# Kernel optimization log

Hardware: AMD Instinct MI355X
Metric: run time of the kernel (lower is better)

## Reference

```python
import jax, jax.numpy as jnp
import numpy as np

N = 4096
INPUT_DIM = 256
HID = 64        # per-head dim == hidden_dim
HEADS = 4
OUT = 256
AIN = 2 * HID   # hidden + positional concat


def sinusoidal_pe(n, d):
    pos = jnp.arange(n, dtype=jnp.float32)[:, None]
    div = jnp.exp(jnp.arange(0, d, 2, dtype=jnp.float32) * (-np.log(10000.0) / d))
    pe = jnp.zeros((n, d), dtype=jnp.float32)
    pe = pe.at[:, 0::2].set(jnp.sin(pos * div))
    pe = pe.at[:, 1::2].set(jnp.cos(pos * div))
    return pe


def layer_norm(x, g, b, eps=1e-5):
    m = x.mean(-1, keepdims=True)
    v = ((x - m) ** 2).mean(-1, keepdims=True)
    return (x - m) / jnp.sqrt(v + eps) * g + b


def setup_inputs() -> dict:
    key = jax.random.key(0)
    ks = jax.random.split(key, 24)
    s = 0.02
    inp = {
        'Z': jax.random.normal(ks[0], (N, INPUT_DIM), jnp.float32),
        'Z_g': jax.random.normal(ks[1], (N, HID), jnp.float32),
        'Z_c': jax.random.normal(ks[2], (N, HID), jnp.float32),
        'adjacency_matrix': jax.random.randint(ks[3], (N, N), 0, 2).astype(jnp.float32),
        'Wq': s * jax.random.normal(ks[4], (AIN, HID * HEADS), jnp.float32),
        'bq': jnp.zeros((HID * HEADS,), jnp.float32),
        'Wk': s * jax.random.normal(ks[5], (AIN, HID * HEADS), jnp.float32),
        'bk': jnp.zeros((HID * HEADS,), jnp.float32),
        'Wv': s * jax.random.normal(ks[6], (AIN, HID * HEADS), jnp.float32),
        'bv': jnp.zeros((HID * HEADS,), jnp.float32),
        'Wo': s * jax.random.normal(ks[7], (HID * HEADS, OUT), jnp.float32),
        'bo': jnp.zeros((OUT,), jnp.float32),
        'Wr': s * jax.random.normal(ks[8], (INPUT_DIM, OUT), jnp.float32),
        'br': jnp.zeros((OUT,), jnp.float32),
        'ln1_g': jnp.ones((OUT,), jnp.float32),
        'ln1_b': jnp.zeros((OUT,), jnp.float32),
        'ln2_g': jnp.ones((OUT,), jnp.float32),
        'ln2_b': jnp.zeros((OUT,), jnp.float32),
        'f1_w': s * jax.random.normal(ks[9], (OUT, OUT * 4), jnp.float32),
        'f1_b': jnp.zeros((OUT * 4,), jnp.float32),
        'f2_w': s * jax.random.normal(ks[10], (OUT * 4, OUT * 2), jnp.float32),
        'f2_b': jnp.zeros((OUT * 2,), jnp.float32),
        'f3_w': s * jax.random.normal(ks[11], (OUT * 2, OUT), jnp.float32),
        'f3_b': jnp.zeros((OUT,), jnp.float32),
        'structure_weight': jnp.asarray(0.1, jnp.float32),
    }
    return inp


def reference(Z, Z_g, Z_c, adjacency_matrix, Wq, bq, Wk, bk, Wv, bv, Wo, bo,
              Wr, br, ln1_g, ln1_b, ln2_g, ln2_b, f1_w, f1_b, f2_w, f2_b,
              f3_w, f3_b, structure_weight):
    n = Z.shape[0]
    pos = sinusoidal_pe(n, HID)                       # [N, HID]
    Zg_p = jnp.concatenate([Z_g, pos], axis=-1)       # [N, 2*HID]
    Zc_p = jnp.concatenate([Z_c, pos], axis=-1)

    Q = (Zc_p @ Wq + bq).reshape(n, HEADS, HID).transpose(1, 0, 2)  # [H,N,D]
    K = (Zg_p @ Wk + bk).reshape(n, HEADS, HID).transpose(1, 0, 2)
    V = (Zg_p @ Wv + bv).reshape(n, HEADS, HID).transpose(1, 0, 2)

    scores = jnp.einsum('hnd,hmd->hnm', Q, K) / jnp.sqrt(jnp.asarray(HID, jnp.float32))
    structure_mask = (adjacency_matrix == 0).astype(jnp.float32) * -1e9  # [N,N]
    scores = scores + structure_weight * structure_mask[None, :, :]

    attn = jax.nn.softmax(scores, axis=-1)            # [H,N,N]
    attended = jnp.einsum('hnm,hmd->hnd', attn, V)    # [H,N,D]
    attended = attended.transpose(1, 0, 2).reshape(n, HEADS * HID)

    out = attended @ Wo + bo
    residual = Z @ Wr + br
    out = layer_norm(out + residual, ln1_g, ln1_b)

    h = jax.nn.gelu(out @ f1_w + f1_b, approximate=False)
    h = jax.nn.gelu(h @ f2_w + f2_b, approximate=False)
    ffn = h @ f3_w + f3_b
    out = layer_norm(out + ffn, ln2_g, ln2_b)
    return out, attn
```

## Files before the change

kernel.cpp:

```cpp
#include <hip/hip_runtime.h>
#include <cmath>

typedef __attribute__((ext_vector_type(8))) short bf16x8;
typedef __attribute__((ext_vector_type(4))) float f32x4;

#define MFMA16(A,B,C) __builtin_amdgcn_mfma_f32_16x16x32_bf16(A,B,C,0,0,0)

__device__ __forceinline__ ushort f2bf(float x){
  union { float f; unsigned u; } v; v.f = x;
  unsigned r = (v.u + 0x7fffu + ((v.u >> 16) & 1u)) >> 16;
  return (ushort)r;
}
__device__ __forceinline__ float bf2f(ushort h){
  union { unsigned u; float f; } v; v.u = ((unsigned)h) << 16;
  return v.f;
}


__global__ __launch_bounds__(256) void k_cvtZ(const float* Z, ushort* AZ){
  int r = blockIdx.x, c = threadIdx.x;
  AZ[(size_t)r*512 + 256 + c] = f2bf(Z[(size_t)r*256 + c]);
}

__global__ __launch_bounds__(256) void k_transpose(const float* in, ushort* out,
                                                   int K, int N, int RS, int CO){
  __shared__ float t[32][33];
  int kb = blockIdx.x*32, nb = blockIdx.y*32;
  int tx = threadIdx.x & 31, ty = threadIdx.x >> 5;
  for (int i = ty; i < 32; i += 8){
    int k = kb + i, n = nb + tx;
    t[i][tx] = (k < K && n < N) ? in[(size_t)k*N + n] : 0.f;
  }
  __syncthreads();
  for (int i = ty; i < 32; i += 8){
    int n = nb + i, k = kb + tx;
    if (n < N && k < K) out[(size_t)n*RS + CO + k] = f2bf(t[tx][i]);
  }
}

__global__ void k_biasor(const float* bo, const float* br, float* out){
  int j = threadIdx.x;
  out[j] = bo[j] + br[j];
}

__global__ __launch_bounds__(256) void k_qkv(
    const float* Zg, const float* Zc,
    const float* Wq, const float* bq, const float* Wk, const float* bk,
    const float* Wv, const float* bv,
    ushort* qb, ushort* kbuf, ushort* vb){
  __shared__ float zcp[16][128], zgp[16][128];
  int r0 = blockIdx.x * 16;
  int t = threadIdx.x;
  for (int i = t; i < 2048; i += 256){
    int row = i >> 7, c = i & 127;
    float vc, vg;
    if (c < 64){
      vc = Zc[(size_t)(r0+row)*64 + c];
      vg = Zg[(size_t)(r0+row)*64 + c];
    } else {
      int ii = (c - 64) >> 1;
      float div = __expf(-0.28782313662425572f * (float)ii);
      float arg = (float)(r0 + row) * div;
      float pe = ((c - 64) & 1) ? cosf(arg) : sinf(arg);
      vc = pe; vg = pe;
    }
    zcp[row][c] = vc; zgp[row][c] = vg;
  }
  __syncthreads();
  float aq[16], ak[16], av[16];
  #pragma unroll
  for (int r = 0; r < 16; r++){ aq[r]=0.f; ak[r]=0.f; av[r]=0.f; }
  int j = t;
  #pragma unroll 4
  for (int k = 0; k < 128; k++){
    float wq = Wq[(size_t)k*256 + j];
    float wk = Wk[(size_t)k*256 + j];
    float wv = Wv[(size_t)k*256 + j];
    #pragma unroll
    for (int r = 0; r < 16; r++){
      float xc = zcp[r][k], xg = zgp[r][k];
      aq[r] = fmaf(xc, wq, aq[r]);
      ak[r] = fmaf(xg, wk, ak[r]);
      av[r] = fmaf(xg, wv, av[r]);
    }
  }
  int h = j >> 6, d = j & 63;
  float bqv = bq[j], bkv = bk[j], bvv = bv[j];
  #pragma unroll
  for (int r = 0; r < 16; r++){
    size_t base = ((size_t)h*4096 + (r0 + r))*64 + d;
    qb[base]   = f2bf((aq[r] + bqv) * 0.125f);
    kbuf[base] = f2bf(ak[r] + bkv);
    vb[base]   = f2bf(av[r] + bvv);
  }
}

__global__ __launch_bounds__(256) void k_vtrans(const ushort* vb, ushort* vtb){
  __shared__ ushort t[64][65];
  int h = blockIdx.y, n0 = blockIdx.x * 64;
  int tx = threadIdx.x & 63, ty = threadIdx.x >> 6;
  for (int i = ty; i < 64; i += 4)
    t[i][tx] = vb[((size_t)h*4096 + n0 + i)*64 + tx];
  __syncthreads();
  for (int i = ty; i < 64; i += 4)
    vtb[((size_t)h*64 + i)*4096 + n0 + tx] = t[tx][i];
}

__global__ __launch_bounds__(512) void k_attn2(
    const ushort* qb, const ushort* kbuf, const ushort* vtb,
    const float* adj, float* attn_out, ushort* az){
  __shared__ ushort pbf[2][16][128];
  __shared__ float  red[8][16];
  __shared__ float  rsl[16];
  __shared__ float  pvp[8][16][33];

  int h  = blockIdx.x >> 8;
  int nb = blockIdx.x & 255;
  int n0 = nb * 16;
  int t = threadIdx.x;
  int wave = t >> 6, lane = t & 63, lr = lane & 15, lg = lane >> 4;
  int srow = t >> 5, sc4 = (t & 31) * 4;

  const ushort* Qh = qb   + ((size_t)h*4096 + n0)*64;
  const ushort* Kh = kbuf + (size_t)h*4096*64;
  const ushort* Vt = vtb  + (size_t)h*64*4096;
  float* aout = attn_out + (size_t)h*4096*4096 + (size_t)n0*4096;

  bf16x8 afr0 = *(const bf16x8*)(Qh + (size_t)lr*64 +  0 + lg*8);
  bf16x8 afr1 = *(const bf16x8*)(Qh + (size_t)lr*64 + 32 + lg*8);

  float rsum[4] = {0.f, 0.f, 0.f, 0.f};
  #pragma unroll 2
  for (int ct = 0; ct < 32; ct++){
    int c0 = ct*128 + wave*16;
    const ushort* kp = Kh + (size_t)(c0+lr)*64 + lg*8;
    bf16x8 b0 = *(const bf16x8*)(kp);
    bf16x8 b1 = *(const bf16x8*)(kp + 32);
    const float* ap = adj + (size_t)(n0 + lg*4)*4096 + c0 + lr;
    float a0 = ap[0], a1 = ap[4096], a2 = ap[8192], a3 = ap[12288];
    f32x4 acc = {0.f, 0.f, 0.f, 0.f};
    acc = MFMA16(afr0, b0, acc);
    acc = MFMA16(afr1, b1, acc);
    rsum[0] += a0 * __expf(acc[0]);
    rsum[1] += a1 * __expf(acc[1]);
    rsum[2] += a2 * __expf(acc[2]);
    rsum[3] += a3 * __expf(acc[3]);
  }
  #pragma unroll
  for (int m = 1; m <= 8; m <<= 1){
    #pragma unroll
    for (int r = 0; r < 4; r++) rsum[r] += __shfl_xor(rsum[r], m, 64);
  }
  if (lr == 0){
    #pragma unroll
    for (int r = 0; r < 4; r++) red[wave][lg*4 + r] = rsum[r];
  }
  __syncthreads();
  if (t < 16){
    float s = 0.f;
    #pragma unroll
    for (int w2 = 0; w2 < 8; w2++) s += red[w2][t];
    rsl[t] = 1.f / s;
  }
  __syncthreads();
  float rs[4];
  #pragma unroll
  for (int r = 0; r < 4; r++) rs[r] = rsl[lg*4 + r];

  int ks = wave & 3;
  int dh = wave >> 2;
  f32x4 pacc[2];
  pacc[0] = (f32x4){0.f,0.f,0.f,0.f};
  pacc[1] = (f32x4){0.f,0.f,0.f,0.f};

  for (int ct = 0; ct < 32; ct++){
    int C0 = ct*128, c0 = C0 + wave*16;
    const ushort* kp = Kh + (size_t)(c0+lr)*64 + lg*8;
    bf16x8 b0 = *(const bf16x8*)(kp);
    bf16x8 b1 = *(const bf16x8*)(kp + 32);
    const float* ap = adj + (size_t)(n0 + lg*4)*4096 + c0 + lr;
    float a0 = ap[0], a1 = ap[4096], a2 = ap[8192], a3 = ap[12288];
    const ushort* vp = Vt + (size_t)(dh*32 + lr)*4096 + C0 + ks*32 + lg*8;
    bf16x8 v0 = *(const bf16x8*)(vp);
    bf16x8 v1 = *(const bf16x8*)(vp + (size_t)16*4096);

    f32x4 acc = {0.f, 0.f, 0.f, 0.f};
    acc = MFMA16(afr0, b0, acc);
    acc = MFMA16(afr1, b1, acc);

    ushort* pb = &pbf[ct & 1][0][0];
    int col = wave*16 + lr;
    float a4[4] = {a0, a1, a2, a3};
    #pragma unroll
    for (int r = 0; r < 4; r++){
      int row = lg*4 + r;
      pb[row*128 + (col ^ ((row & 7) << 3))] = f2bf(a4[r] * __expf(acc[r]) * rs[r]);
    }
    __syncthreads();

    bf16x8 pa = *(const bf16x8*)(pb + lr*128 + ((ks*32 + lg*8) ^ ((lr & 7) << 3)));
    pacc[0] = MFMA16(pa, v0, pacc[0]);
    pacc[1] = MFMA16(pa, v1, pacc[1]);

    const ushort* src = pb + srow*128 + (sc4 ^ ((srow & 7) << 3));
    ushort s4[4];
    *(uint2*)s4 = *(const uint2*)src;
    f32x4 ov = {bf2f(s4[0]), bf2f(s4[1]), bf2f(s4[2]), bf2f(s4[3])};
    __builtin_nontemporal_store(ov, (f32x4*)(aout + (size_t)srow*4096 + C0 + sc4));
  }

  #pragma unroll
  for (int dfl = 0; dfl < 2; dfl++)
    #pragma unroll
    for (int r = 0; r < 4; r++)
      pvp[wave][lg*4 + r][dfl*16 + lr] = pacc[dfl][r];
  __syncthreads();
  {
    int row = t >> 5;
    int d2  = (t & 31) * 2;
    union { ushort u[2]; uint q; } pk;
    #pragma unroll
    for (int e = 0; e < 2; e++){
      int d = d2 + e, dhh = d >> 5, dl = d & 31;
      float s = pvp[dhh*4+0][row][dl] + pvp[dhh*4+1][row][dl]
              + pvp[dhh*4+2][row][dl] + pvp[dhh*4+3][row][dl];
      pk.u[e] = f2bf(s);
    }
    *(uint*)(az + (size_t)(n0 + row)*512 + h*64 + d2) = pk.q;
  }
}

__global__ __launch_bounds__(256) void k_gemm(
    const ushort* A, const ushort* Bt, const float* bias,
    const float* res, float* outf, ushort* outb,
    int M, int N, int K, int mode){
  __shared__ __align__(16) ushort la[64][40];
  __shared__ __align__(16) ushort lb[64][40];
  int mb = blockIdx.x * 64, nb = blockIdx.y * 64;
  int t = threadIdx.x;
  int wave = t >> 6, lane = t & 63, lr = lane & 15, lg = lane >> 4;
  int wm = (wave >> 1) * 32, wn = (wave & 1) * 32;
  f32x4 acc[2][2];
  #pragma unroll
  for (int i = 0; i < 2; i++)
    #pragma unroll
    for (int j = 0; j < 2; j++) acc[i][j] = (f32x4){0.f,0.f,0.f,0.f};

  int srow = t >> 2, scol = (t & 3) * 8;
  for (int k0 = 0; k0 < K; k0 += 32){
    *(bf16x8*)&la[srow][scol] = *(const bf16x8*)(A  + (size_t)(mb+srow)*K + k0 + scol);
    *(bf16x8*)&lb[srow][scol] = *(const bf16x8*)(Bt + (size_t)(nb+srow)*K + k0 + scol);
    __syncthreads();
    #pragma unroll
    for (int i = 0; i < 2; i++){
      bf16x8 af = *(const bf16x8*)&la[wm + i*16 + lr][lg*8];
      #pragma unroll
      for (int j = 0; j < 2; j++){
        bf16x8 bfg = *(const bf16x8*)&lb[wn + j*16 + lr][lg*8];
        acc[i][j] = MFMA16(af, bfg, acc[i][j]);
      }
    }
    __syncthreads();
  }

  #pragma unroll
  for (int i = 0; i < 2; i++)
    #pragma unroll
    for (int j = 0; j < 2; j++){
      int col = nb + wn + j*16 + lr;
      float bv = bias[col];
      #pragma unroll
      for (int r = 0; r < 4; r++){
        int row = mb + wm + i*16 + lg*4 + r;
        float v = acc[i][j][r] + bv;
        if (mode == 0){
          if (res) v += res[(size_t)row*N + col];
          outf[(size_t)row*N + col] = v;
        } else {
          float gl = 0.5f * v * (1.f + erff(v * 0.70710678118f));
          outb[(size_t)row*N + col] = f2bf(gl);
        }
      }
    }
}

__global__ __launch_bounds__(256) void k_ln(const float* X, const float* g, const float* b,
                                            float* outf, ushort* outb){
  int row = blockIdx.x * 4 + (threadIdx.x >> 6);
  int lane = threadIdx.x & 63;
  const float* xr = X + (size_t)row*256;
  f32x4 v = *(const f32x4*)(xr + lane*4);
  float s = v[0] + v[1] + v[2] + v[3];
  #pragma unroll
  for (int m = 32; m >= 1; m >>= 1) s += __shfl_xor(s, m, 64);
  float mean = s * (1.f/256.f);
  float d0[4]; float sq = 0.f;
  #pragma unroll
  for (int e = 0; e < 4; e++){ d0[e] = v[e] - mean; sq += d0[e]*d0[e]; }
  #pragma unroll
  for (int m = 32; m >= 1; m >>= 1) sq += __shfl_xor(sq, m, 64);
  float rstd = rsqrtf(sq * (1.f/256.f) + 1e-5f);
  float o[4];
  #pragma unroll
  for (int e = 0; e < 4; e++)
    o[e] = d0[e]*rstd*g[lane*4 + e] + b[lane*4 + e];
  if (outf){
    f32x4 ov = {o[0], o[1], o[2], o[3]};
    *(f32x4*)(outf + (size_t)row*256 + lane*4) = ov;
  }
  if (outb){
    union { ushort u[4]; uint2 q; } pk;
    #pragma unroll
    for (int e = 0; e < 4; e++) pk.u[e] = f2bf(o[e]);
    *(uint2*)(outb + (size_t)row*256 + lane*4) = pk.q;
  }
}

extern "C" void kernel_launch(void* const* d_in, const int* in_sizes, int n_in,
                              void* d_out, int out_size, void* d_ws, size_t ws_size,
                              hipStream_t stream){
  const float* Z    = (const float*)d_in[0];
  const float* Zg   = (const float*)d_in[1];
  const float* Zc   = (const float*)d_in[2];
  const float* adj  = (const float*)d_in[3];
  const float* Wq   = (const float*)d_in[4];
  const float* bq   = (const float*)d_in[5];
  const float* Wk   = (const float*)d_in[6];
  const float* bk   = (const float*)d_in[7];
  const float* Wv   = (const float*)d_in[8];
  const float* bv   = (const float*)d_in[9];
  const float* Wo   = (const float*)d_in[10];
  const float* bo   = (const float*)d_in[11];
  const float* Wr   = (const float*)d_in[12];
  const float* br   = (const float*)d_in[13];
  const float* ln1g = (const float*)d_in[14];
  const float* ln1b = (const float*)d_in[15];
  const float* ln2g = (const float*)d_in[16];
  const float* ln2b = (const float*)d_in[17];
  const float* f1w  = (const float*)d_in[18];
  const float* f1b  = (const float*)d_in[19];
  const float* f2w  = (const float*)d_in[20];
  const float* f2b  = (const float*)d_in[21];
  const float* f3w  = (const float*)d_in[22];
  const float* f3b  = (const float*)d_in[23];

  float* outF  = (float*)d_out;
  float* attnF = outF + (size_t)4096*256;

  const size_t MB = 1048576;
  char* w = (char*)d_ws;
  ushort* qb    = (ushort*)(w + 0*MB);
  ushort* kbuf  = (ushort*)(w + 2*MB);
  ushort* vtb   = (ushort*)(w + 4*MB);
  ushort* vb    = (ushort*)(w + 6*MB);
  ushort* h1    = (ushort*)(w + 0*MB);
  ushort* AZ    = (ushort*)(w + 8*MB);
  ushort* h2    = (ushort*)(w + 8*MB);
  ushort* BoR   = (ushort*)(w + 12*MB);
  float*  biasOR= (float*)(w + 12*MB + 262144);
  ushort* f1T   = (ushort*)(w + 13*MB);
  ushort* f2T   = (ushort*)(w + 13*MB + 524288);
  ushort* f3T   = (ushort*)(w + 14*MB + 524288);
  float*  X1    = (float*)(w + 15*MB);
  float*  yf    = (float*)(w + 19*MB);
  ushort* yb    = (ushort*)(w + 23*MB);

  k_cvtZ<<<4096, 256, 0, stream>>>(Z, AZ);
  k_transpose<<<dim3(8,  8), 256, 0, stream>>>(Wo,  BoR,  256,  256, 512,   0);
  k_transpose<<<dim3(8,  8), 256, 0, stream>>>(Wr,  BoR,  256,  256, 512, 256);
  k_transpose<<<dim3(8, 32), 256, 0, stream>>>(f1w, f1T,  256, 1024, 256,   0);
  k_transpose<<<dim3(32,16), 256, 0, stream>>>(f2w, f2T, 1024,  512, 1024,  0);
  k_transpose<<<dim3(16, 8), 256, 0, stream>>>(f3w, f3T,  512,  256, 512,   0);
  k_biasor<<<1, 256, 0, stream>>>(bo, br, biasOR);

  k_qkv<<<256, 256, 0, stream>>>(Zg, Zc, Wq, bq, Wk, bk, Wv, bv, qb, kbuf, vb);
  k_vtrans<<<dim3(64, 4), 256, 0, stream>>>(vb, vtb);

  k_attn2<<<1024, 512, 0, stream>>>(qb, kbuf, vtb, adj, attnF, AZ);

  k_gemm<<<dim3(64, 4), 256, 0, stream>>>(AZ, BoR, biasOR, nullptr, X1, nullptr,
                                          4096, 256, 512, 0);
  k_ln<<<1024, 256, 0, stream>>>(X1, ln1g, ln1b, yf, yb);

  k_gemm<<<dim3(64,16), 256, 0, stream>>>(yb, f1T, f1b, nullptr, nullptr, h1,
                                          4096, 1024, 256, 1);
  k_gemm<<<dim3(64, 8), 256, 0, stream>>>(h1, f2T, f2b, nullptr, nullptr, h2,
                                          4096, 512, 1024, 1);
  k_gemm<<<dim3(64, 4), 256, 0, stream>>>(h2, f3T, f3b, yf, X1, nullptr,
                                          4096, 256, 512, 0);
  k_ln<<<1024, 256, 0, stream>>>(X1, ln2g, ln2b, outF, nullptr);
}
```

Baseline: 327.6 us.

## Remove per-tile block barrier in attention PV pass via per-wave P tiles

The PV pass no longer shares a block-wide P tile behind a __syncthreads on every column tile. Each wave now keeps its own 16x16 P fragment in wave-private LDS and multiplies it against all 64 V dims, using a zero-padded half-K MFMA. Partial outputs from the 8 waves are reduced at the end. The attn matrix is written straight from registers as fp32 instead of being read back from bf16 LDS. K, adjacency and V loads are software-prefetched one iteration ahead, and launch bounds request 4 blocks per CU. The cost is wasted MFMA work from the half-zero K operand, a larger final reduction and scalar rather than vectorised attn stores. Written attn values are no longer bf16-rounded.

```diff
diff --git a/kernel.cpp b/kernel.cpp
--- a/kernel.cpp
+++ b/kernel.cpp
@@ -106,20 +106,19 @@
     vtb[((size_t)h*64 + i)*4096 + n0 + tx] = t[tx][i];
 }
 
-__global__ __launch_bounds__(512) void k_attn2(
+__global__ __launch_bounds__(512, 4) void k_attn2(
     const ushort* qb, const ushort* kbuf, const ushort* vtb,
     const float* adj, float* attn_out, ushort* az){
-  __shared__ ushort pbf[2][16][128];
+  __shared__ ushort pw[8][16][16];
   __shared__ float  red[8][16];
   __shared__ float  rsl[16];
-  __shared__ float  pvp[8][16][33];
+  __shared__ float  pvp[8][16][68];
 
   int h  = blockIdx.x >> 8;
   int nb = blockIdx.x & 255;
   int n0 = nb * 16;
   int t = threadIdx.x;
   int wave = t >> 6, lane = t & 63, lr = lane & 15, lg = lane >> 4;
-  int srow = t >> 5, sc4 = (t & 31) * 4;
 
   const ushort* Qh = qb   + ((size_t)h*4096 + n0)*64;
   const ushort* Kh = kbuf + (size_t)h*4096*64;
@@ -129,22 +128,31 @@
   bf16x8 afr0 = *(const bf16x8*)(Qh + (size_t)lr*64 +  0 + lg*8);
   bf16x8 afr1 = *(const bf16x8*)(Qh + (size_t)lr*64 + 32 + lg*8);
 
+  const ushort* kp0 = Kh  + (size_t)(wave*16 + lr)*64 + lg*8;
+  const float*  ap0 = adj + (size_t)(n0 + lg*4)*4096 + wave*16 + lr;
+
   float rsum[4] = {0.f, 0.f, 0.f, 0.f};
-  #pragma unroll 2
+  bf16x8 b0c = *(const bf16x8*)(kp0);
+  bf16x8 b1c = *(const bf16x8*)(kp0 + 32);
+  float a0c = ap0[0], a1c = ap0[4096], a2c = ap0[8192], a3c = ap0[12288];
   for (int ct = 0; ct < 32; ct++){
-    int c0 = ct*128 + wave*16;
-    const ushort* kp = Kh + (size_t)(c0+lr)*64 + lg*8;
-    bf16x8 b0 = *(const bf16x8*)(kp);
-    bf16x8 b1 = *(const bf16x8*)(kp + 32);
-    const float* ap = adj + (size_t)(n0 + lg*4)*4096 + c0 + lr;
-    float a0 = ap[0], a1 = ap[4096], a2 = ap[8192], a3 = ap[12288];
+    int ctn = ct < 31 ? ct + 1 : 31;
+    const ushort* kpn = kp0 + (size_t)ctn*8192;
+    const float*  apn = ap0 + (size_t)ctn*128;
+    bf16x8 b0n = *(const bf16x8*)(kpn);
+    bf16x8 b1n = *(const bf16x8*)(kpn + 32);
+    float a0n = apn[0], a1n = apn[4096], a2n = apn[8192], a3n = apn[12288];
+
     f32x4 acc = {0.f, 0.f, 0.f, 0.f};
-    acc = MFMA16(afr0, b0, acc);
-    acc = MFMA16(afr1, b1, acc);
-    rsum[0] += a0 * __expf(acc[0]);
-    rsum[1] += a1 * __expf(acc[1]);
-    rsum[2] += a2 * __expf(acc[2]);
-    rsum[3] += a3 * __expf(acc[3]);
+    acc = MFMA16(afr0, b0c, acc);
+    acc = MFMA16(afr1, b1c, acc);
+    rsum[0] += a0c * __expf(acc[0]);
+    rsum[1] += a1c * __expf(acc[1]);
+    rsum[2] += a2c * __expf(acc[2]);
+    rsum[3] += a3c * __expf(acc[3]);
+
+    b0c = b0n; b1c = b1n;
+    a0c = a0n; a1c = a1n; a2c = a2n; a3c = a3n;
   }
   #pragma unroll
   for (int m = 1; m <= 8; m <<= 1){
@@ -167,53 +175,74 @@
   #pragma unroll
   for (int r = 0; r < 4; r++) rs[r] = rsl[lg*4 + r];
 
-  int ks = wave & 3;
-  int dh = wave >> 2;
-  f32x4 pacc[2];
-  pacc[0] = (f32x4){0.f,0.f,0.f,0.f};
-  pacc[1] = (f32x4){0.f,0.f,0.f,0.f};
+  const ushort* vp0 = Vt + (size_t)lr*4096 + wave*16 + 8*(lg & 1);
+  int lgLow = (lg < 2);
+
+  f32x4 pacc[4];
+  #pragma unroll
+  for (int d = 0; d < 4; d++) pacc[d] = (f32x4){0.f,0.f,0.f,0.f};
+
+  b0c = *(const bf16x8*)(kp0);
+  b1c = *(const bf16x8*)(kp0 + 32);
+  a0c = ap0[0]; a1c = ap0[4096]; a2c = ap0[8192]; a3c = ap0[12288];
+  bf16x8 v0c = *(const bf16x8*)(vp0);
+  bf16x8 v1c = *(const bf16x8*)(vp0 + (size_t)16*4096);
+  bf16x8 v2c = *(const bf16x8*)(vp0 + (size_t)32*4096);
+  bf16x8 v3c = *(const bf16x8*)(vp0 + (size_t)48*4096);
 
   for (int ct = 0; ct < 32; ct++){
-    int C0 = ct*128, c0 = C0 + wave*16;
-    const ushort* kp = Kh + (size_t)(c0+lr)*64 + lg*8;
-    bf16x8 b0 = *(const bf16x8*)(kp);
-    bf16x8 b1 = *(const bf16x8*)(kp + 32);
-    const float* ap = adj + (size_t)(n0 + lg*4)*4096 + c0 + lr;
-    float a0 = ap[0], a1 = ap[4096], a2 = ap[8192], a3 = ap[12288];
-    const ushort* vp = Vt + (size_t)(dh*32 + lr)*4096 + C0 + ks*32 + lg*8;
-    bf16x8 v0 = *(const bf16x8*)(vp);
-    bf16x8 v1 = *(const bf16x8*)(vp + (size_t)16*4096);
+    int ctn = ct < 31 ? ct + 1 : 31;
+    const ushort* kpn = kp0 + (size_t)ctn*8192;
+    const float*  apn = ap0 + (size_t)ctn*128;
+    const ushort* vpn = vp0 + (size_t)ctn*128;
+    bf16x8 b0n = *(const bf16x8*)(kpn);
+    bf16x8 b1n = *(const bf16x8*)(kpn + 32);
+    float a0n = apn[0], a1n = apn[4096], a2n = apn[8192], a3n = apn[12288];
+    bf16x8 v0n = *(const bf16x8*)(vpn);
+    bf16x8 v1n = *(const bf16x8*)(vpn + (size_t)16*4096);
+    bf16x8 v2n = *(const bf16x8*)(vpn + (size_t)32*4096);
+    bf16x8 v3n = *(const bf16x8*)(vpn + (size_t)48*4096);
 
     f32x4 acc = {0.f, 0.f, 0.f, 0.f};
-    acc = MFMA16(afr0, b0, acc);
-    acc = MFMA16(afr1, b1, acc);
-
-    ushort* pb = &pbf[ct & 1][0][0];
-    int col = wave*16 + lr;
-    float a4[4] = {a0, a1, a2, a3};
-    #pragma unroll
-    for (int r = 0; r < 4; r++){
-      int row = lg*4 + r;
-      pb[row*128 + (col ^ ((row & 7) << 3))] = f2bf(a4[r] * __expf(acc[r]) * rs[r]);
-    }
-    __syncthreads();
-
-    bf16x8 pa = *(const bf16x8*)(pb + lr*128 + ((ks*32 + lg*8) ^ ((lr & 7) << 3)));
-    pacc[0] = MFMA16(pa, v0, pacc[0]);
-    pacc[1] = MFMA16(pa, v1, pacc[1]);
-
-    const ushort* src = pb + srow*128 + (sc4 ^ ((srow & 7) << 3));
-    ushort s4[4];
-    *(uint2*)s4 = *(const uint2*)src;
-    f32x4 ov = {bf2f(s4[0]), bf2f(s4[1]), bf2f(s4[2]), bf2f(s4[3])};
-    __builtin_nontemporal_store(ov, (f32x4*)(aout + (size_t)srow*4096 + C0 + sc4));
-  }
-
-  #pragma unroll
-  for (int dfl = 0; dfl < 2; dfl++)
+    acc = MFMA16(afr0, b0c, acc);
+    acc = MFMA16(afr1, b1c, acc);
+
+    float pv0 = a0c * __expf(acc[0]) * rs[0];
+    float pv1 = a1c * __expf(acc[1]) * rs[1];
+    float pv2 = a2c * __expf(acc[2]) * rs[2];
+    float pv3 = a3c * __expf(acc[3]) * rs[3];
+
+    int c0 = ct*128 + wave*16;
+    float* ao = aout + (size_t)(lg*4)*4096 + c0 + lr;
+    ao[0]     = pv0;
+    ao[4096]  = pv1;
+    ao[8192]  = pv2;
+    ao[12288] = pv3;
+
+    pw[wave][lg*4 + 0][lr] = f2bf(pv0);
+    pw[wave][lg*4 + 1][lr] = f2bf(pv1);
+    pw[wave][lg*4 + 2][lr] = f2bf(pv2);
+    pw[wave][lg*4 + 3][lr] = f2bf(pv3);
+
+    bf16x8 pa = *(const bf16x8*)&pw[wave][lr][8*(lg & 1)];
+    bf16x8 z8 = {0,0,0,0,0,0,0,0};
+    pa = lgLow ? pa : z8;
+
+    pacc[0] = MFMA16(pa, v0c, pacc[0]);
+    pacc[1] = MFMA16(pa, v1c, pacc[1]);
+    pacc[2] = MFMA16(pa, v2c, pacc[2]);
+    pacc[3] = MFMA16(pa, v3c, pacc[3]);
+
+    b0c = b0n; b1c = b1n;
+    a0c = a0n; a1c = a1n; a2c = a2n; a3c = a3n;
+    v0c = v0n; v1c = v1n; v2c = v2n; v3c = v3n;
+  }
+
+  #pragma unroll
+  for (int df = 0; df < 4; df++)
     #pragma unroll
     for (int r = 0; r < 4; r++)
-      pvp[wave][lg*4 + r][dfl*16 + lr] = pacc[dfl][r];
+      pvp[wave][lg*4 + r][df*16 + lr] = pacc[df][r];
   __syncthreads();
   {
     int row = t >> 5;
@@ -221,9 +250,10 @@
     union { ushort u[2]; uint q; } pk;
     #pragma unroll
     for (int e = 0; e < 2; e++){
-      int d = d2 + e, dhh = d >> 5, dl = d & 31;
-      float s = pvp[dhh*4+0][row][dl] + pvp[dhh*4+1][row][dl]
-              + pvp[dhh*4+2][row][dl] + pvp[dhh*4+3][row][dl];
+      int d = d2 + e;
+      float s = 0.f;
+      #pragma unroll
+      for (int w2 = 0; w2 < 8; w2++) s += pvp[w2][row][d];
       pk.u[e] = f2bf(s);
     }
     *(uint*)(az + (size_t)(n0 + row)*512 + h*64 + d2) = pk.q;
```

After: 410.5 us. +25.3%, slower.

## Restructure attention PV pass into 1024-column chunks with fewer barriers and XCD-aware block mapping

Applied to the files above, without the earlier changes.

The second attention pass now computes probabilities for 1024 columns per chunk into a larger shared buffer, synchronizing twice per chunk instead of once per 128 columns. Each wave then does a full-D PV MFMA over its own 128-column slice rather than splitting D and K across waves. Output stores are reorganized per row, and block indices are remapped so that all four heads for a row block land on the same XCD to share adjacency reads in L2. Shared memory is reused between the P buffer and the final reduction buffer, with launch bounds asking for four blocks per CU. The cost is more registers for the accumulators and loads, and the cross-wave reduction now sums eight partials.

```diff
diff --git a/kernel.cpp b/kernel.cpp
--- a/kernel.cpp
+++ b/kernel.cpp
@@ -106,20 +106,23 @@
     vtb[((size_t)h*64 + i)*4096 + n0 + tx] = t[tx][i];
 }
 
-__global__ __launch_bounds__(512) void k_attn2(
+__global__ __launch_bounds__(512, 4) void k_attn2(
     const ushort* qb, const ushort* kbuf, const ushort* vtb,
     const float* adj, float* attn_out, ushort* az){
-  __shared__ ushort pbf[2][16][128];
-  __shared__ float  red[8][16];
-  __shared__ float  rsl[16];
-  __shared__ float  pvp[8][16][33];
-
-  int h  = blockIdx.x >> 8;
-  int nb = blockIdx.x & 255;
+  __shared__ __align__(16) char smem[8*16*66*4];
+  __shared__ float red[8][16];
+  __shared__ float rsl[16];
+  ushort* pbf = (ushort*)smem;
+  float (*pvp)[16][66] = (float(*)[16][66])smem;
+
+  int bid = blockIdx.x;
+  int xcd = bid & 7, slot = bid >> 3;
+  int nb = xcd*32 + (slot >> 2);
+  int h  = slot & 3;
   int n0 = nb * 16;
+
   int t = threadIdx.x;
   int wave = t >> 6, lane = t & 63, lr = lane & 15, lg = lane >> 4;
-  int srow = t >> 5, sc4 = (t & 31) * 4;
 
   const ushort* Qh = qb   + ((size_t)h*4096 + n0)*64;
   const ushort* Kh = kbuf + (size_t)h*4096*64;
@@ -129,14 +132,16 @@
   bf16x8 afr0 = *(const bf16x8*)(Qh + (size_t)lr*64 +  0 + lg*8);
   bf16x8 afr1 = *(const bf16x8*)(Qh + (size_t)lr*64 + 32 + lg*8);
 
+  const ushort* kp0 = Kh  + (size_t)(wave*16 + lr)*64 + lg*8;
+  const float*  ap0 = adj + (size_t)(n0 + lg*4)*4096 + wave*16 + lr;
+
   float rsum[4] = {0.f, 0.f, 0.f, 0.f};
   #pragma unroll 2
   for (int ct = 0; ct < 32; ct++){
-    int c0 = ct*128 + wave*16;
-    const ushort* kp = Kh + (size_t)(c0+lr)*64 + lg*8;
+    const ushort* kp = kp0 + (size_t)ct*8192;
+    const float*  ap = ap0 + (size_t)ct*128;
     bf16x8 b0 = *(const bf16x8*)(kp);
     bf16x8 b1 = *(const bf16x8*)(kp + 32);
-    const float* ap = adj + (size_t)(n0 + lg*4)*4096 + c0 + lr;
     float a0 = ap[0], a1 = ap[4096], a2 = ap[8192], a3 = ap[12288];
     f32x4 acc = {0.f, 0.f, 0.f, 0.f};
     acc = MFMA16(afr0, b0, acc);
@@ -167,53 +172,67 @@
   #pragma unroll
   for (int r = 0; r < 4; r++) rs[r] = rsl[lg*4 + r];
 
-  int ks = wave & 3;
-  int dh = wave >> 2;
-  f32x4 pacc[2];
-  pacc[0] = (f32x4){0.f,0.f,0.f,0.f};
-  pacc[1] = (f32x4){0.f,0.f,0.f,0.f};
-
-  for (int ct = 0; ct < 32; ct++){
-    int C0 = ct*128, c0 = C0 + wave*16;
-    const ushort* kp = Kh + (size_t)(c0+lr)*64 + lg*8;
-    bf16x8 b0 = *(const bf16x8*)(kp);
-    bf16x8 b1 = *(const bf16x8*)(kp + 32);
-    const float* ap = adj + (size_t)(n0 + lg*4)*4096 + c0 + lr;
-    float a0 = ap[0], a1 = ap[4096], a2 = ap[8192], a3 = ap[12288];
-    const ushort* vp = Vt + (size_t)(dh*32 + lr)*4096 + C0 + ks*32 + lg*8;
-    bf16x8 v0 = *(const bf16x8*)(vp);
-    bf16x8 v1 = *(const bf16x8*)(vp + (size_t)16*4096);
-
-    f32x4 acc = {0.f, 0.f, 0.f, 0.f};
-    acc = MFMA16(afr0, b0, acc);
-    acc = MFMA16(afr1, b1, acc);
-
-    ushort* pb = &pbf[ct & 1][0][0];
-    int col = wave*16 + lr;
-    float a4[4] = {a0, a1, a2, a3};
-    #pragma unroll
-    for (int r = 0; r < 4; r++){
-      int row = lg*4 + r;
-      pb[row*128 + (col ^ ((row & 7) << 3))] = f2bf(a4[r] * __expf(acc[r]) * rs[r]);
+  f32x4 pacc[4];
+  #pragma unroll
+  for (int d = 0; d < 4; d++) pacc[d] = (f32x4){0.f,0.f,0.f,0.f};
+
+  for (int ct = 0; ct < 4; ct++){
+    int C0 = ct * 1024;
+
+    #pragma unroll
+    for (int s = 0; s < 8; s++){
+      int cw = s*128 + wave*16;
+      const ushort* kp = Kh + (size_t)(C0 + cw + lr)*64 + lg*8;
+      const float*  ap = adj + (size_t)(n0 + lg*4)*4096 + C0 + cw + lr;
+      bf16x8 b0 = *(const bf16x8*)(kp);
+      bf16x8 b1 = *(const bf16x8*)(kp + 32);
+      float a0 = ap[0], a1 = ap[4096], a2 = ap[8192], a3 = ap[12288];
+      f32x4 acc = {0.f, 0.f, 0.f, 0.f};
+      acc = MFMA16(afr0, b0, acc);
+      acc = MFMA16(afr1, b1, acc);
+      float a4[4] = {a0, a1, a2, a3};
+      int col = cw + lr;
+      #pragma unroll
+      for (int r = 0; r < 4; r++){
+        int row = lg*4 + r;
+        pbf[row*1024 + (col ^ ((row & 7) << 3))] = f2bf(a4[r] * __expf(acc[r]) * rs[r]);
+      }
     }
     __syncthreads();
 
-    bf16x8 pa = *(const bf16x8*)(pb + lr*128 + ((ks*32 + lg*8) ^ ((lr & 7) << 3)));
-    pacc[0] = MFMA16(pa, v0, pacc[0]);
-    pacc[1] = MFMA16(pa, v1, pacc[1]);
-
-    const ushort* src = pb + srow*128 + (sc4 ^ ((srow & 7) << 3));
-    ushort s4[4];
-    *(uint2*)s4 = *(const uint2*)src;
-    f32x4 ov = {bf2f(s4[0]), bf2f(s4[1]), bf2f(s4[2]), bf2f(s4[3])};
-    __builtin_nontemporal_store(ov, (f32x4*)(aout + (size_t)srow*4096 + C0 + sc4));
-  }
-
-  #pragma unroll
-  for (int dfl = 0; dfl < 2; dfl++)
+    #pragma unroll
+    for (int ks = 0; ks < 4; ks++){
+      int kb2 = wave*128 + ks*32;
+      bf16x8 pa = *(const bf16x8*)&pbf[lr*1024 + ((kb2 + lg*8) ^ ((lr & 7) << 3))];
+      #pragma unroll
+      for (int df = 0; df < 4; df++){
+        bf16x8 v8 = *(const bf16x8*)(Vt + (size_t)(df*16 + lr)*4096 + C0 + kb2 + lg*8);
+        pacc[df] = MFMA16(pa, v8, pacc[df]);
+      }
+    }
+
+    #pragma unroll
+    for (int rr = 0; rr < 2; rr++){
+      int row = wave*2 + rr;
+      int swz = (row & 7) << 3;
+      #pragma unroll
+      for (int q = 0; q < 4; q++){
+        int c = q*256 + lane*4;
+        const ushort* src = &pbf[row*1024 + (c ^ swz)];
+        ushort s4[4];
+        *(uint2*)s4 = *(const uint2*)src;
+        f32x4 ov = {bf2f(s4[0]), bf2f(s4[1]), bf2f(s4[2]), bf2f(s4[3])};
+        __builtin_nontemporal_store(ov, (f32x4*)(aout + (size_t)row*4096 + C0 + c));
+      }
+    }
+    __syncthreads();
+  }
+
+  #pragma unroll
+  for (int df = 0; df < 4; df++)
     #pragma unroll
     for (int r = 0; r < 4; r++)
-      pvp[wave][lg*4 + r][dfl*16 + lr] = pacc[dfl][r];
+      pvp[wave][lg*4 + r][df*16 + lr] = pacc[df][r];
   __syncthreads();
   {
     int row = t >> 5;
@@ -221,9 +240,10 @@
     union { ushort u[2]; uint q; } pk;
     #pragma unroll
     for (int e = 0; e < 2; e++){
-      int d = d2 + e, dhh = d >> 5, dl = d & 31;
-      float s = pvp[dhh*4+0][row][dl] + pvp[dhh*4+1][row][dl]
-              + pvp[dhh*4+2][row][dl] + pvp[dhh*4+3][row][dl];
+      int d = d2 + e;
+      float s = 0.f;
+      #pragma unroll
+      for (int w2 = 0; w2 < 8; w2++) s += pvp[w2][row][d];
       pk.u[e] = f2bf(s);
     }
     *(uint*)(az + (size_t)(n0 + row)*512 + h*64 + d2) = pk.q;
```

New measurement: 340.2 us. 1.04x slower.
